# Kernel optimization log

Hardware: AMD Instinct MI355X
Metric: run time of the kernel (lower is better)

The kernel has to match this reference:

```python
import jax, jax.numpy as jnp
from jax import lax
import numpy as np
import math

IN_SHAPE = [2, 4, 4]   # factorize(32, 4)
OUT_SHAPE = [2, 4, 4]
RANK = 8
GROUPS = 1
KH = KW = 3
OUT_CH = 32
IN_CH = 32


def setup_inputs() -> dict:
    key = jax.random.key(0)
    ks = jax.random.split(key, 6)

    def uni(k, shape, bound):
        return jax.random.uniform(k, shape, jnp.float32, -bound, bound)

    kernels = []
    for l in range(3):
        fi, fo = IN_SHAPE[l], OUT_SHAPE[l]
        bound = math.sqrt(6.0 / (fi + fo))
        kernels.append(uni(ks[l], (IN_SHAPE[l], OUT_SHAPE[l], RANK), bound))
    bound = math.sqrt(6.0 / (KH * KW * RANK + KH * KW))
    k3 = uni(ks[3], (GROUPS, KH, KW, RANK), bound)

    x = jax.random.normal(ks[4], (8, IN_CH, 512, 512), dtype=jnp.float32)
    bias = jnp.zeros((OUT_CH,), dtype=jnp.float32)
    return {"x": x, "k0": kernels[0], "k1": kernels[1], "k2": kernels[2],
            "k3": k3, "bias": bias}


def reference(x, k0, k1, k2, k3, bias):
    # CP weight reconstruction (chained einsums, as in the torch module)
    wl = jnp.einsum('iar,jbr->ijabr', k0, k1)          # [2,2,4,4,R]
    wr = jnp.einsum('kcr,ghwr->ghwkcr', k2, k3)        # [1,3,3,4,4,R]
    w = jnp.einsum('ijabr,ghwkcr->gijkabchw', wl, wr)  # [1,2,4,4,2,4,4,3,3]
    w = w.reshape(OUT_CH, IN_CH // GROUPS, KH, KW)     # [O, I, 3, 3]
    # flip + true convolution in conv_einsum == cross-correlation with w;
    # 'max'-mode output then [1:-1] trim == valid conv of the pad-1 input.
    out = lax.conv_general_dilated(
        x, w, window_strides=(1, 1), padding=((1, 1), (1, 1)),
        dimension_numbers=('NCHW', 'OIHW', 'NCHW'),
        feature_group_count=GROUPS)
    out = out + bias[None, :, None, None]
    return out  # [batch, out_channels, 512, 512]
```

## Files before the change

kernel.cpp:

```cpp
#include <hip/hip_runtime.h>
#include <hip/hip_bf16.h>

#define H 512
#define W 512
#define C 32
#define O 32
#define TW 64
#define SH 16
#define NS 4
#define RING 12
#define XCOLS (TW + 2)

using bf16x8 = __attribute__((ext_vector_type(8))) short;
using f32x4  = __attribute__((ext_vector_type(4))) float;

__device__ __forceinline__ unsigned short f2bf(float f) {
    union { float f; unsigned u; } c; c.f = f;
    unsigned r = c.u + 0x7fffu + ((c.u >> 16) & 1u);
    return (unsigned short)(r >> 16);
}

__device__ __forceinline__ uint4 pack8(const float* v) {
    uint4 pk;
    pk.x = (unsigned)f2bf(v[0]) | ((unsigned)f2bf(v[1]) << 16);
    pk.y = (unsigned)f2bf(v[2]) | ((unsigned)f2bf(v[3]) << 16);
    pk.z = (unsigned)f2bf(v[4]) | ((unsigned)f2bf(v[5]) << 16);
    pk.w = (unsigned)f2bf(v[6]) | ((unsigned)f2bf(v[7]) << 16);
    return pk;
}

__global__ void recon_w(const float* __restrict__ k0, const float* __restrict__ k1,
                        const float* __restrict__ k2, const float* __restrict__ k3,
                        unsigned short* __restrict__ wout) {
    int idx = blockIdx.x * 256 + threadIdx.x;
    if (idx >= 9 * 32 * 32) return;
    int ci = idx & 31;
    int o  = (idx >> 5) & 31;
    int s  = idx >> 10;
    int i = o >> 4, j = (o >> 2) & 3, k = o & 3;
    int a = ci >> 4, b = (ci >> 2) & 3, c = ci & 3;
    float acc = 0.f;
    #pragma unroll
    for (int r = 0; r < 8; ++r)
        acc += k0[(i*2 + a)*8 + r] * k1[(j*4 + b)*8 + r]
             * k2[(k*4 + c)*8 + r] * k3[s*8 + r];
    wout[idx] = f2bf(acc);
}

__launch_bounds__(256, 3)
__global__ void conv_mfma(const float* __restrict__ x,
                          const unsigned short* __restrict__ wq,
                          const float* __restrict__ bias,
                          float* __restrict__ out) {
    __shared__ __align__(16) unsigned short sx[RING][XCOLS][C];

    const int tid = threadIdx.x;
    const int bid = ((blockIdx.x & 7) << 8) | (blockIdx.x >> 3);
    const int n  = bid >> 8;
    const int ty = (bid >> 3) & 31;
    const int tx = bid & 7;
    const int y0 = ty * SH, x0 = tx * TW;

    const int lane = tid & 63;
    const int wave = tid >> 6;
    const int pix  = lane & 15;
    const int quad = lane >> 4;

    bf16x8 bw[9][2];
    #pragma unroll
    for (int s = 0; s < 9; ++s)
        #pragma unroll
        for (int h = 0; h < 2; ++h)
            bw[s][h] = *(const bf16x8*)(wq + ((s*32 + h*16 + pix)*32 + quad*8));

    for (int task = tid; task < 6 * 4 * XCOLS; task += 256) {
        int gxl = task % XCOLS;
        int t2  = task / XCOLS;
        int ciq = t2 & 3;
        int r   = t2 >> 2;
        int gy = y0 - 1 + r;
        int gx = x0 + gxl - 1;
        bool inb = (gy >= 0) && (gx >= 0) && (gx < W);
        const float* p = x + (((n*C + ciq*8)*H + gy)*W + gx);
        float v[8];
        #pragma unroll
        for (int j2 = 0; j2 < 8; ++j2) v[j2] = inb ? p[j2 * H * W] : 0.f;
        int pos = ciq ^ ((gxl >> 1) & 3);
        *(uint4*)&sx[r][gxl][pos * 8] = pack8(v);
    }
    __syncthreads();

    const float b0 = bias[pix];
    const float b1 = bias[16 + pix];

    int rbase = 0;
    for (int s = 0; s < NS; ++s) {
        const bool more = (s + 1 < NS);

        float v[4][8];
        float vh[8];
        int hcol = 0, hciq = 0, hrow = 0;
        if (more) {
            #pragma unroll
            for (int k = 0; k < 4; ++k) {
                int gy = y0 + 4*s + 5 + k;
                bool inb = (gy < H);
                const float* p = x + (((n*C + wave*8)*H + gy)*W + x0 + lane);
                #pragma unroll
                for (int j2 = 0; j2 < 8; ++j2)
                    v[k][j2] = inb ? p[j2 * H * W] : 0.f;
            }
            if (tid < 32) {
                hcol = (tid & 1) ? (XCOLS - 1) : 0;
                hciq = (tid >> 1) & 3;
                hrow = tid >> 3;
                int gy = y0 + 4*s + 5 + hrow;
                int gx = x0 + hcol - 1;
                bool inb = (gy < H) && (gx >= 0) && (gx < W);
                const float* p = x + (((n*C + hciq*8)*H + gy)*W + gx);
                #pragma unroll
                for (int j2 = 0; j2 < 8; ++j2)
                    vh[j2] = inb ? p[j2 * H * W] : 0.f;
            }
        }
        __builtin_amdgcn_sched_barrier(0);

        const int gy_out = y0 + 4*s + wave;
        #pragma unroll
        for (int mt = 0; mt < 4; ++mt) {
            const int xm = mt << 4;
            f32x4 acc0 = {0.f, 0.f, 0.f, 0.f};
            f32x4 acc1 = {0.f, 0.f, 0.f, 0.f};
            __builtin_amdgcn_s_setprio(1);
            #pragma unroll
            for (int stp = 0; stp < 9; ++stp) {
                const int dy = stp / 3, dx = stp % 3;
                int sl = rbase + wave + dy; if (sl >= RING) sl -= RING;
                const int xp = xm + pix + dx;
                const int pos = quad ^ ((xp >> 1) & 3);
                bf16x8 a = *(const bf16x8*)&sx[sl][xp][pos * 8];
                acc0 = __builtin_amdgcn_mfma_f32_16x16x32_bf16(a, bw[stp][0], acc0, 0, 0, 0);
                acc1 = __builtin_amdgcn_mfma_f32_16x16x32_bf16(a, bw[stp][1], acc1, 0, 0, 0);
            }
            __builtin_amdgcn_s_setprio(0);
            const int base0 = ((n*O + pix     ) * H + gy_out) * W + x0 + xm + quad*4;
            const int base1 = ((n*O + 16 + pix) * H + gy_out) * W + x0 + xm + quad*4;
            f32x4 o0 = acc0 + b0;
            f32x4 o1 = acc1 + b1;
            *(f32x4*)(out + base0) = o0;
            *(f32x4*)(out + base1) = o1;
        }

        if (more) {
            #pragma unroll
            for (int k = 0; k < 4; ++k) {
                int sl = rbase + 6 + k; if (sl >= RING) sl -= RING;
                int gxl = lane + 1;
                int pos = wave ^ ((gxl >> 1) & 3);
                *(uint4*)&sx[sl][gxl][pos * 8] = pack8(v[k]);
            }
            if (tid < 32) {
                int sl = rbase + 6 + hrow; if (sl >= RING) sl -= RING;
                int pos = hciq ^ ((hcol >> 1) & 3);
                *(uint4*)&sx[sl][hcol][pos * 8] = pack8(vh);
            }
            __syncthreads();
        }

        rbase += 4; if (rbase >= RING) rbase -= RING;
    }
}

extern "C" void kernel_launch(void* const* d_in, const int* in_sizes, int n_in,
                              void* d_out, int out_size, void* d_ws, size_t ws_size,
                              hipStream_t stream) {
    const float* x    = (const float*)d_in[0];
    const float* k0   = (const float*)d_in[1];
    const float* k1   = (const float*)d_in[2];
    const float* k2   = (const float*)d_in[3];
    const float* k3   = (const float*)d_in[4];
    const float* bias = (const float*)d_in[5];
    float* out = (float*)d_out;
    unsigned short* wbuf = (unsigned short*)d_ws;

    recon_w<<<36, 256, 0, stream>>>(k0, k1, k2, k3, wbuf);
    conv_mfma<<<2048, 256, 0, stream>>>(x, wbuf, bias, out);
}
```

Measured before the change: 483.3 us.

## Pre-convert input to padded NHWC bf16 and convolve directly from global

Adds a pre-pass kernel that transposes the NCHW fp32 input into a zero-padded NHWC bf16 buffer in workspace. A new conv kernel then loads its 3x3 MFMA operands straight from global/cache with no LDS ring, no in-kernel conversion and no barriers. The original LDS-ring kernel is kept as a fallback when the workspace is too small. The trade-off is an extra full pass over the input (read fp32, write bf16) plus redundant global reads of overlapping halo rows, in exchange for a simpler conv loop.

```diff
diff --git a/kernel.cpp b/kernel.cpp
--- a/kernel.cpp
+++ b/kernel.cpp
@@ -5,6 +5,10 @@
 #define W 512
 #define C 32
 #define O 32
+#define YP (H + 2)
+#define XPD (W + 2)
+#define ROWS 16
+
 #define TW 64
 #define SH 16
 #define NS 4
@@ -47,6 +51,88 @@
     wout[idx] = f2bf(acc);
 }
 
+__launch_bounds__(256)
+__global__ void to_nhwc(const float* __restrict__ x,
+                        unsigned short* __restrict__ xp) {
+    const int bid = blockIdx.x;
+    const int n  = bid / YP;
+    const int yy = bid - n * YP;
+    const int gy = yy - 1;
+    for (int t = threadIdx.x; t < XPD * 4; t += 256) {
+        int ciq = t & 3;
+        int xx  = t >> 2;
+        int gx = xx - 1;
+        bool inb = (gx >= 0) && (gx < W) && (gy >= 0) && (gy < H);
+        const float* p = x + (((n*C + ciq*8)*H + gy)*W + gx);
+        float v[8];
+        #pragma unroll
+        for (int j = 0; j < 8; ++j) v[j] = inb ? p[j * H * W] : 0.f;
+        *(uint4*)&xp[(((n*YP + yy))*XPD + xx)*32 + ciq*8] = pack8(v);
+    }
+}
+
+__launch_bounds__(256, 3)
+__global__ void conv_nhwc(const unsigned short* __restrict__ xp,
+                          const unsigned short* __restrict__ wq,
+                          const float* __restrict__ bias,
+                          float* __restrict__ out) {
+    const int tid = threadIdx.x;
+    const int bid = ((blockIdx.x & 7) << 8) | (blockIdx.x >> 3);
+    const int n  = bid >> 8;
+    const int yb = (bid >> 3) & 31;
+    const int xb = bid & 7;
+    const int y0 = yb * ROWS, x0 = xb * 64;
+
+    const int lane = tid & 63;
+    const int wave = tid >> 6;
+    const int pix  = lane & 15;
+    const int quad = lane >> 4;
+    const int xs   = x0 + wave * 16;
+
+    bf16x8 bw[9][2];
+    #pragma unroll
+    for (int s = 0; s < 9; ++s)
+        #pragma unroll
+        for (int h = 0; h < 2; ++h)
+            bw[s][h] = *(const bf16x8*)(wq + ((s*32 + h*16 + pix)*32 + quad*8));
+
+    const float b0 = bias[pix];
+    const float b1 = bias[16 + pix];
+
+    for (int r = 0; r < ROWS; ++r) {
+        const int gy = y0 + r;
+        const unsigned short* ap =
+            xp + (((n*YP + gy))*XPD + xs + pix)*32 + quad*8;
+
+        bf16x8 a[3][3];
+        #pragma unroll
+        for (int dy = 0; dy < 3; ++dy)
+            #pragma unroll
+            for (int dx = 0; dx < 3; ++dx)
+                a[dy][dx] = *(const bf16x8*)(ap + (dy*XPD + dx)*32);
+
+        f32x4 acc0 = {0.f, 0.f, 0.f, 0.f};
+        f32x4 acc1 = {0.f, 0.f, 0.f, 0.f};
+        __builtin_amdgcn_s_setprio(1);
+        #pragma unroll
+        for (int dy = 0; dy < 3; ++dy)
+            #pragma unroll
+            for (int dx = 0; dx < 3; ++dx) {
+                const int stp = dy*3 + dx;
+                acc0 = __builtin_amdgcn_mfma_f32_16x16x32_bf16(a[dy][dx], bw[stp][0], acc0, 0, 0, 0);
+                acc1 = __builtin_amdgcn_mfma_f32_16x16x32_bf16(a[dy][dx], bw[stp][1], acc1, 0, 0, 0);
+            }
+        __builtin_amdgcn_s_setprio(0);
+
+        const int base0 = ((n*O + pix     ) * H + gy) * W + xs + quad*4;
+        const int base1 = ((n*O + 16 + pix) * H + gy) * W + xs + quad*4;
+        f32x4 o0 = acc0 + b0;
+        f32x4 o1 = acc1 + b1;
+        *(f32x4*)(out + base0) = o0;
+        *(f32x4*)(out + base1) = o1;
+    }
+}
+
 __launch_bounds__(256, 3)
 __global__ void conv_mfma(const float* __restrict__ x,
                           const unsigned short* __restrict__ wq,
@@ -96,7 +182,6 @@
     int rbase = 0;
     for (int s = 0; s < NS; ++s) {
         const bool more = (s + 1 < NS);
-
         float v[4][8];
         float vh[8];
         int hcol = 0, hciq = 0, hrow = 0;
@@ -136,9 +221,9 @@
             for (int stp = 0; stp < 9; ++stp) {
                 const int dy = stp / 3, dx = stp % 3;
                 int sl = rbase + wave + dy; if (sl >= RING) sl -= RING;
-                const int xp = xm + pix + dx;
-                const int pos = quad ^ ((xp >> 1) & 3);
-                bf16x8 a = *(const bf16x8*)&sx[sl][xp][pos * 8];
+                const int xp2 = xm + pix + dx;
+                const int pos = quad ^ ((xp2 >> 1) & 3);
+                bf16x8 a = *(const bf16x8*)&sx[sl][xp2][pos * 8];
                 acc0 = __builtin_amdgcn_mfma_f32_16x16x32_bf16(a, bw[stp][0], acc0, 0, 0, 0);
                 acc1 = __builtin_amdgcn_mfma_f32_16x16x32_bf16(a, bw[stp][1], acc1, 0, 0, 0);
             }
@@ -184,5 +269,14 @@
     unsigned short* wbuf = (unsigned short*)d_ws;
 
     recon_w<<<36, 256, 0, stream>>>(k0, k1, k2, k3, wbuf);
-    conv_mfma<<<2048, 256, 0, stream>>>(x, wbuf, bias, out);
-}
+
+    const size_t nhwc_bytes = (size_t)8 * YP * XPD * 32 * 2;
+    const size_t need = 32768 + nhwc_bytes;
+    if (ws_size >= need) {
+        unsigned short* xph = (unsigned short*)((char*)d_ws + 32768);
+        to_nhwc<<<8 * YP, 256, 0, stream>>>(x, xph);
+        conv_nhwc<<<2048, 256, 0, stream>>>(xph, wbuf, bias, out);
+    } else {
+        conv_mfma<<<2048, 256, 0, stream>>>(x, wbuf, bias, out);
+    }
+}
```

After: 595.1 us. 23.1% more time.
